# Kernel optimization log

Measured on AMD Instinct MI355X. Metric: run time of the kernel, lower is better.

## Reference

```python
import jax, jax.numpy as jnp
import numpy as np

N, E, G, ND, H, C, L = 100000, 640000, 1000, 128, 128, 10, 4
ATOMS_PER_GRAPH = 100  # N = G * ATOMS_PER_GRAPH
NEG_SLOPE = 0.01  # nn.LeakyReLU default


def setup_inputs() -> dict:
    key = jax.random.key(0)
    ks = jax.random.split(key, 16)
    s = 0.05
    return {
        "node_attr": jax.random.normal(ks[0], (N, ND), jnp.float32),
        "edge_index": jax.random.randint(ks[1], (2, E), 0, N, jnp.int64),
        "num_atoms": jnp.full((G,), ATOMS_PER_GRAPH, dtype=jnp.int64),
        "enc_W": jax.random.normal(ks[2], (ND, H), jnp.float32) * s,
        "enc_b": jnp.zeros((H,), jnp.float32),
        "gcn_W": jax.random.normal(ks[3], (L, H, H), jnp.float32) * s,
        "gcn_b": jnp.zeros((L, H), jnp.float32),
        "r_W1": jax.random.normal(ks[4], (H, H), jnp.float32) * s,
        "r_b1": jnp.zeros((H,), jnp.float32),
        "r_W2": jax.random.normal(ks[5], (H, H), jnp.float32) * s,
        "r_b2": jnp.zeros((H,), jnp.float32),
        "s_W1": jax.random.normal(ks[6], (H, H), jnp.float32) * s,
        "s_b1": jnp.zeros((H,), jnp.float32),
        "s_W2": jax.random.normal(ks[7], (H, H), jnp.float32) * s,
        "s_b2": jnp.zeros((H,), jnp.float32),
        "fin_W": jax.random.normal(ks[8], (H, C), jnp.float32) * s,
        "fin_b": jnp.zeros((C,), jnp.float32),
    }


def _leaky(x):
    return jnp.where(x > 0, x, NEG_SLOPE * x)


def reference(node_attr, edge_index, num_atoms, enc_W, enc_b, gcn_W, gcn_b,
              r_W1, r_b1, r_W2, r_b2, s_W1, s_b1, s_W2, s_b2, fin_W, fin_b):
    dst, src = edge_index[0], edge_index[1]
    # degree normalization constant across layers: deg(i) = in-edge count, divide by deg+1
    deg = jax.ops.segment_sum(jnp.ones((E,), node_attr.dtype), dst, num_segments=N)
    inv_deg = 1.0 / (deg + 1.0)  # [N]

    x = node_attr @ enc_W + enc_b  # [N, H]
    for l in range(L):
        h = x @ gcn_W[l] + gcn_b[l]
        agg = jax.ops.segment_sum(h[src], dst, num_segments=N)  # scatter_sum over dst
        x = (h + agg) * inv_deg[:, None]

    # GateMLP: ReLuMLP(x) * SigmoidMLP(x)
    r = _leaky(_leaky(x @ r_W1 + r_b1) @ r_W2 + r_b2)
    g = jax.nn.sigmoid(_leaky(x @ s_W1 + s_b1) @ s_W2 + s_b2)
    x = r * g  # [N, H]

    # graph pooling: scatter_mean over graph ids
    graph_mask = jnp.repeat(jnp.arange(G), num_atoms, total_repeat_length=N)
    gsum = jax.ops.segment_sum(x, graph_mask, num_segments=G)
    cnt = jax.ops.segment_sum(jnp.ones((N,), x.dtype), graph_mask, num_segments=G)
    graph_attr = gsum / jnp.maximum(cnt, 1.0)[:, None]  # [G, H]
    return graph_attr @ fin_W + fin_b  # [G, C]
```

## Files before the change

kernel.cpp:

```cpp
#include <hip/hip_runtime.h>
#include <hip/hip_bf16.h>
#include <cstddef>
#include <cstdint>

#define CAP 32
#define LEAK 0.01f

typedef __attribute__((ext_vector_type(8))) short short8v;
typedef __attribute__((ext_vector_type(4))) float float4v;

__device__ __forceinline__ unsigned short f2bf(float f) {
    uint32_t u = __float_as_uint(f);
    uint32_t r = (u + 0x7FFFu + ((u >> 16) & 1u)) >> 16;
    return (unsigned short)r;
}
__device__ __forceinline__ float bf2f(unsigned short s) {
    return __uint_as_float(((uint32_t)s) << 16);
}
__device__ __forceinline__ short8v frag_from_pairs(uint32_t p0, uint32_t p1,
                                                   uint32_t p2, uint32_t p3) {
    union { uint32_t u[4]; short8v v; } c;
    c.u[0] = p0; c.u[1] = p1; c.u[2] = p2; c.u[3] = p3;
    return c.v;
}

__global__ __launch_bounds__(256) void prep(const int* __restrict__ ei, int E_,
                                            int* __restrict__ cnt,
                                            int* __restrict__ bucket,
                                            const float* __restrict__ node_attr,
                                            unsigned short* __restrict__ bx, int Nn,
                                            const float* __restrict__ enc_W,
                                            const float* __restrict__ gcn_W,
                                            const float* __restrict__ rw1,
                                            const float* __restrict__ rw2,
                                            const float* __restrict__ sw1,
                                            const float* __restrict__ sw2,
                                            const float* __restrict__ enc_b,
                                            const float* __restrict__ gcn_b,
                                            const float* __restrict__ rb1,
                                            const float* __restrict__ sb1,
                                            unsigned short* __restrict__ wpack,
                                            float* __restrict__ fbias,
                                            const int* __restrict__ na,
                                            int* __restrict__ goff, int G_,
                                            int NB_EDGE, int NB_CVT) {
    const int b = blockIdx.x;
    const int tid = threadIdx.x;

    if (b < NB_EDGE) {
        int e = (b * 256 + tid) * 4;
        if (e >= E_) return;
        if (e + 4 <= E_) {
            int4 d4 = *(const int4*)&ei[e];
            int4 s4 = *(const int4*)&ei[(size_t)E_ + e];
            int p0 = atomicAdd(&cnt[d4.x], 1);
            int p1 = atomicAdd(&cnt[d4.y], 1);
            int p2 = atomicAdd(&cnt[d4.z], 1);
            int p3 = atomicAdd(&cnt[d4.w], 1);
            if (p0 < CAP) bucket[(size_t)d4.x * CAP + p0] = s4.x;
            if (p1 < CAP) bucket[(size_t)d4.y * CAP + p1] = s4.y;
            if (p2 < CAP) bucket[(size_t)d4.z * CAP + p2] = s4.z;
            if (p3 < CAP) bucket[(size_t)d4.w * CAP + p3] = s4.w;
        } else {
            for (; e < E_; ++e) {
                int d = ei[e], s = ei[(size_t)E_ + e];
                int p = atomicAdd(&cnt[d], 1);
                if (p < CAP) bucket[(size_t)d * CAP + p] = s;
            }
        }
        return;
    }
    if (b < NB_EDGE + NB_CVT) {
        size_t i8 = ((size_t)(b - NB_EDGE) * 256 + tid) * 8;
        if (i8 < (size_t)Nn * 128) {
            const float* ap = node_attr + i8;
            float4v p = *(const float4v*)ap;
            float4v q = *(const float4v*)(ap + 4);
            short8v v;
            v[0] = (short)f2bf(p[0]); v[1] = (short)f2bf(p[1]);
            v[2] = (short)f2bf(p[2]); v[3] = (short)f2bf(p[3]);
            v[4] = (short)f2bf(q[0]); v[5] = (short)f2bf(q[1]);
            v[6] = (short)f2bf(q[2]); v[7] = (short)f2bf(q[3]);
            *(short8v*)(bx + i8) = v;
        }
        return;
    }
    if (b < NB_EDGE + NB_CVT + 72) {
        int pb = b - (NB_EDGE + NB_CVT);
        int m = pb >> 3;
        if (m == 1) return;
        int idx = (pb & 7) * 256 + tid;
        const float* W;
        switch (m) {
            case 0: W = enc_W; break;
            case 2: case 3: case 4: W = gcn_W + (size_t)(m - 1) * 16384; break;
            case 5: W = rw1; break;
            case 6: W = rw2; break;
            case 7: W = sw1; break;
            default: W = sw2; break;
        }
        int n = idx & 127;
        int fg = (idx >> 7) & 3;
        int kc = idx >> 9;
        short8v v;
#pragma unroll
        for (int j = 0; j < 8; ++j)
            v[j] = (short)f2bf(W[(size_t)(kc * 32 + fg * 8 + j) * 128 + n]);
        *(short8v*)(wpack + (size_t)m * 16384 + (size_t)idx * 8) = v;
        return;
    }
    int fb = b - (NB_EDGE + NB_CVT + 72);
    if (fb < 192) {
        int which = fb / 64;
        int r = (fb % 64) * 2 + (tid >> 7);
        int n = tid & 127;
        const float* A = (which == 0) ? enc_W : gcn_W + (size_t)3 * 16384;
        const float* B = (which == 0) ? gcn_W : ((which == 1) ? rw1 : sw1);
        float acc = 0.f;
#pragma unroll 8
        for (int m2 = 0; m2 < 128; ++m2)
            acc = fmaf(A[(size_t)r * 128 + m2], B[(size_t)m2 * 128 + n], acc);
        int kc = r >> 5, fg2 = (r >> 3) & 3, j = r & 7;
        int sl = (which == 0) ? 1 : ((which == 1) ? 9 : 10);
        wpack[(size_t)sl * 16384 + (size_t)(((kc * 4 + fg2) * 128 + n) * 8 + j)] = f2bf(acc);
    } else if (fb < 195) {
        if (tid < 128) {
            int which = fb - 192;
            const float* B = (which == 0) ? gcn_W : ((which == 1) ? rw1 : sw1);
            const float* ba = (which == 0) ? enc_b : gcn_b + 384;
            const float* bb = (which == 0) ? gcn_b : ((which == 1) ? rb1 : sb1);
            float acc = bb[tid];
            for (int m2 = 0; m2 < 128; ++m2)
                acc = fmaf(ba[m2], B[(size_t)m2 * 128 + tid], acc);
            fbias[which * 128 + tid] = acc;
        }
    } else if (fb == 195) {
        __shared__ int sh[256];
        int base = tid * 4;
        int v0 = (base + 0 < G_) ? na[base + 0] : 0;
        int v1 = (base + 1 < G_) ? na[base + 1] : 0;
        int v2 = (base + 2 < G_) ? na[base + 2] : 0;
        int v3 = (base + 3 < G_) ? na[base + 3] : 0;
        int s = v0 + v1 + v2 + v3;
        sh[tid] = s;
        __syncthreads();
        for (int ofs = 1; ofs < 256; ofs <<= 1) {
            int u = (tid >= ofs) ? sh[tid - ofs] : 0;
            __syncthreads();
            sh[tid] += u;
            __syncthreads();
        }
        int run = sh[tid] - s;
        if (tid == 0) goff[0] = 0;
        run += v0; if (base + 0 < G_) goff[base + 1] = run;
        run += v1; if (base + 1 < G_) goff[base + 2] = run;
        run += v2; if (base + 2 < G_) goff[base + 3] = run;
        run += v3; if (base + 3 < G_) goff[base + 4] = run;
    }
}

__device__ __forceinline__ void load_wf(const unsigned short* __restrict__ Wpack,
                                        int w, int fr, int fg, short8v wf[2][4]) {
    const short8v* Wp = (const short8v*)Wpack;
#pragma unroll
    for (int t = 0; t < 2; ++t)
#pragma unroll
        for (int kc = 0; kc < 4; ++kc)
            wf[t][kc] = Wp[(kc * 4 + fg) * 128 + w * 32 + t * 16 + fr];
}

__device__ __forceinline__ void mfma_tile(const unsigned short* As, int fr, int fg,
                                          const short8v wf[2][4], float4v acc[4][2]) {
#pragma unroll
    for (int m = 0; m < 4; ++m) {
        acc[m][0] = (float4v){0.f, 0.f, 0.f, 0.f};
        acc[m][1] = (float4v){0.f, 0.f, 0.f, 0.f};
    }
#pragma unroll
    for (int kc = 0; kc < 4; ++kc) {
        short8v a[4];
#pragma unroll
        for (int m = 0; m < 4; ++m) {
            int row = m * 16 + fr;
            int cb = (kc * 64 + fg * 16) ^ ((row & 7) << 4);
            a[m] = *(const short8v*)((const char*)As + row * 256 + cb);
        }
#pragma unroll
        for (int m = 0; m < 4; ++m) {
            acc[m][0] = __builtin_amdgcn_mfma_f32_16x16x32_bf16(a[m], wf[0][kc], acc[m][0], 0, 0, 0);
            acc[m][1] = __builtin_amdgcn_mfma_f32_16x16x32_bf16(a[m], wf[1][kc], acc[m][1], 0, 0, 0);
        }
    }
}

__device__ __forceinline__ void acc8(float a[8], uint4 v, float m) {
    a[0] = fmaf(m, bf2f((unsigned short)(v.x & 0xffff)), a[0]);
    a[1] = fmaf(m, bf2f((unsigned short)(v.x >> 16)), a[1]);
    a[2] = fmaf(m, bf2f((unsigned short)(v.y & 0xffff)), a[2]);
    a[3] = fmaf(m, bf2f((unsigned short)(v.y >> 16)), a[3]);
    a[4] = fmaf(m, bf2f((unsigned short)(v.z & 0xffff)), a[4]);
    a[5] = fmaf(m, bf2f((unsigned short)(v.z >> 16)), a[5]);
    a[6] = fmaf(m, bf2f((unsigned short)(v.w & 0xffff)), a[6]);
    a[7] = fmaf(m, bf2f((unsigned short)(v.w >> 16)), a[7]);
}

__device__ __forceinline__ void issue4(const char* __restrict__ xb, int2 prep_,
                                       int gl, int l16, int Nn, int jb, uint4 V[4]) {
    const int sl = gl + (jb >> 1);
    int s0 = __shfl(prep_.x, sl);
    int s1 = __shfl(prep_.y, sl);
    int s2 = __shfl(prep_.x, sl + 1);
    int s3 = __shfl(prep_.y, sl + 1);
    s0 = min(max(s0, 0), Nn - 1);
    s1 = min(max(s1, 0), Nn - 1);
    s2 = min(max(s2, 0), Nn - 1);
    s3 = min(max(s3, 0), Nn - 1);
    V[0] = *(const uint4*)(xb + (size_t)s0 * 256 + l16 * 16);
    V[1] = *(const uint4*)(xb + (size_t)s1 * 256 + l16 * 16);
    V[2] = *(const uint4*)(xb + (size_t)s2 * 256 + l16 * 16);
    V[3] = *(const uint4*)(xb + (size_t)s3 * 256 + l16 * 16);
}

__device__ __forceinline__ void consume4(float a[8], const uint4 V[4], int jb, int d) {
    acc8(a, V[0], (jb + 0 < d) ? 1.f : 0.f);
    acc8(a, V[1], (jb + 1 < d) ? 1.f : 0.f);
    acc8(a, V[2], (jb + 2 < d) ? 1.f : 0.f);
    acc8(a, V[3], (jb + 3 < d) ? 1.f : 0.f);
}

template <bool AGGONLY>
__global__ __launch_bounds__(256, 4) void gcn_fused(const unsigned short* __restrict__ x,
                                                    const int* __restrict__ bucket,
                                                    const int* __restrict__ cnt,
                                                    const unsigned short* __restrict__ Wpack,
                                                    const float* __restrict__ bias,
                                                    unsigned short* __restrict__ xout,
                                                    int Nn) {
    __shared__ unsigned short As[64 * 128];
    const int tid = threadIdx.x;
    const int lane = tid & 63;
    const int w = tid >> 6;
    const int row0 = blockIdx.x * 64;
    const int fr = lane & 15;
    const int fg = lane >> 4;
    const int l16 = lane & 15;
    const int g = lane >> 4;
    const int gl = lane & 48;
    const char* xb = (const char*)x;

    int cfull = 0;
    if (lane < 16) {
        int gn = row0 + w * 16 + lane;
        if (gn >= Nn) gn = Nn - 1;
        cfull = cnt[gn];
    }
    uint4 own[4];
    int2 pre[4];
#pragma unroll
    for (int p = 0; p < 4; ++p) {
        int gn = row0 + w * 16 + p * 4 + g;
        if (gn >= Nn) gn = Nn - 1;
        own[p] = *(const uint4*)(xb + (size_t)gn * 256 + l16 * 16);
        pre[p] = *(const int2*)&bucket[(size_t)gn * CAP + 2 * l16];
    }

#pragma unroll
    for (int p = 0; p < 4; ++p) {
        const int n = p * 4 + g;
        const int r = w * 16 + n;
        const int dfull = __shfl(cfull, n);
        const float id = 1.0f / (float)(dfull + 1);
        const int d = min(dfull, CAP);

        uint4 VA[4], VB[4];
        issue4(xb, pre[p], gl, l16, Nn, 0, VA);

        float a[8];
        {
            uint4 o = own[p];
            a[0] = bf2f((unsigned short)(o.x & 0xffff));
            a[1] = bf2f((unsigned short)(o.x >> 16));
            a[2] = bf2f((unsigned short)(o.y & 0xffff));
            a[3] = bf2f((unsigned short)(o.y >> 16));
            a[4] = bf2f((unsigned short)(o.z & 0xffff));
            a[5] = bf2f((unsigned short)(o.z >> 16));
            a[6] = bf2f((unsigned short)(o.w & 0xffff));
            a[7] = bf2f((unsigned short)(o.w >> 16));
        }

        int j = 0;
        while (true) {
            if (j + 4 < d) issue4(xb, pre[p], gl, l16, Nn, j + 4, VB);
            consume4(a, VA, j, d);
            j += 4;
            if (j >= d) break;
            if (j + 4 < d) issue4(xb, pre[p], gl, l16, Nn, j + 4, VA);
            consume4(a, VB, j, d);
            j += 4;
            if (j >= d) break;
        }

#pragma unroll
        for (int i = 0; i < 8; ++i) a[i] *= id;
        uint4 o;
        o.x = (uint32_t)f2bf(a[0]) | ((uint32_t)f2bf(a[1]) << 16);
        o.y = (uint32_t)f2bf(a[2]) | ((uint32_t)f2bf(a[3]) << 16);
        o.z = (uint32_t)f2bf(a[4]) | ((uint32_t)f2bf(a[5]) << 16);
        o.w = (uint32_t)f2bf(a[6]) | ((uint32_t)f2bf(a[7]) << 16);
        if (AGGONLY) {
            int node = row0 + r;
            if (node < Nn)
                *(uint4*)((char*)xout + (size_t)node * 256 + l16 * 16) = o;
        } else {
            *(uint4*)((char*)As + r * 256 + ((l16 * 16) ^ ((r & 7) << 4))) = o;
        }
    }
    if (AGGONLY) return;

    short8v wf[2][4];
    load_wf(Wpack, w, fr, fg, wf);
    __syncthreads();

    float4v acc[4][2];
    mfma_tile(As, fr, fg, wf, acc);

#pragma unroll
    for (int t = 0; t < 2; ++t) {
        const int col = w * 32 + t * 16 + fr;
        const float bv = bias[col];
#pragma unroll
        for (int m = 0; m < 4; ++m)
#pragma unroll
            for (int q = 0; q < 4; ++q) {
                int row = row0 + m * 16 + fg * 4 + q;
                if (row < Nn) xout[(size_t)row * 128 + col] = f2bf(acc[m][t][q] + bv);
            }
    }
}

__global__ __launch_bounds__(512, 4) void gate_fused(const unsigned short* __restrict__ x,
                                                     const unsigned short* __restrict__ wpack,
                                                     const float* __restrict__ rb1f,
                                                     const float* __restrict__ rb2,
                                                     const float* __restrict__ sb1f,
                                                     const float* __restrict__ sb2,
                                                     unsigned short* __restrict__ out, int M) {
    __shared__ unsigned short Ws[2 * 128 * 128];
    const int tid = threadIdx.x;
    const int lane = tid & 63;
    const int w = tid >> 6;
    const int l16 = lane & 15;
    const int fg = lane >> 4;
    const int row0 = blockIdx.x * 128 + w * 16;

    int xr = row0 + l16;
    if (xr >= M) xr = M - 1;
    short8v xbf[4];
#pragma unroll
    for (int kc = 0; kc < 4; ++kc)
        xbf[kc] = *(const short8v*)(x + (size_t)xr * 128 + kc * 32 + fg * 8);

    const short8v* WL = (const short8v*)Ws;
    uint32_t upR[8][2], upS[8][2];

#define STAGE2(mi0, mi1)                                                      \
    {                                                                         \
        const short8v* s0 = (const short8v*)(wpack + (size_t)(mi0) * 16384);  \
        const short8v* s1 = (const short8v*)(wpack + (size_t)(mi1) * 16384);  \
        short8v* dst = (short8v*)Ws;                                          \
        _Pragma("unroll") for (int i = 0; i < 4; ++i)                         \
            dst[i * 512 + tid] = s0[i * 512 + tid];                          \
        _Pragma("unroll") for (int i = 0; i < 4; ++i)                         \
            dst[2048 + i * 512 + tid] = s1[i * 512 + tid];                    \
    }

#define PASS1(OFS, BIAS, UP)                                                  \
    _Pragma("unroll") for (int nt = 0; nt < 8; ++nt) {                        \
        float4v acc = (float4v){0.f, 0.f, 0.f, 0.f};                          \
        _Pragma("unroll") for (int kc = 0; kc < 4; ++kc)                      \
            acc = __builtin_amdgcn_mfma_f32_16x16x32_bf16(                    \
                WL[(OFS) + (kc * 4 + fg) * 128 + nt * 16 + l16], xbf[kc], acc, 0, 0, 0); \
        _Pragma("unroll") for (int q = 0; q < 4; ++q) {                       \
            float v = acc[q] + (BIAS)[nt * 16 + fg * 4 + q];                  \
            acc[q] = v > 0.f ? v : LEAK * v;                                  \
        }                                                                     \
        UP[nt][0] = (uint32_t)f2bf(acc[0]) | ((uint32_t)f2bf(acc[1]) << 16);  \
        UP[nt][1] = (uint32_t)f2bf(acc[2]) | ((uint32_t)f2bf(acc[3]) << 16);  \
    }

#define MKUF(UP, UF)                                                          \
    _Pragma("unroll") for (int kc = 0; kc < 4; ++kc) {                        \
        uint32_t pr0, pr1, pr2, pr3;                                          \
        {                                                                     \
            int srcl = (((2 * fg + 0) & 3) << 4) + l16;                       \
            uint32_t lo = __shfl((int)UP[2 * kc][0], srcl);                   \
            uint32_t hi = __shfl((int)UP[2 * kc + 1][0], srcl);               \
            pr0 = (fg & 2) ? hi : lo;                                         \
            lo = __shfl((int)UP[2 * kc][1], srcl);                            \
            hi = __shfl((int)UP[2 * kc + 1][1], srcl);                        \
            pr1 = (fg & 2) ? hi : lo;                                         \
        }                                                                     \
        {                                                                     \
            int srcl = (((2 * fg + 1) & 3) << 4) + l16;                       \
            uint32_t lo = __shfl((int)UP[2 * kc][0], srcl);                   \
            uint32_t hi = __shfl((int)UP[2 * kc + 1][0], srcl);               \
            pr2 = (fg & 2) ? hi : lo;                                         \
            lo = __shfl((int)UP[2 * kc][1], srcl);                            \
            hi = __shfl((int)UP[2 * kc + 1][1], srcl);                        \
            pr3 = (fg & 2) ? hi : lo;                                         \
        }                                                                     \
        UF[kc] = frag_from_pairs(pr0, pr1, pr2, pr3);                         \
    }

    STAGE2(9, 10);
    __syncthreads();
    PASS1(0, rb1f, upR);
    PASS1(2048, sb1f, upS);
    __syncthreads();

    STAGE2(6, 8);
    __syncthreads();

    short8v uf[4];
    MKUF(upR, uf);
    float4v rf[8];
#pragma unroll
    for (int t2 = 0; t2 < 8; ++t2) {
        float4v acc = (float4v){0.f, 0.f, 0.f, 0.f};
#pragma unroll
        for (int kc = 0; kc < 4; ++kc)
            acc = __builtin_amdgcn_mfma_f32_16x16x32_bf16(
                uf[kc], WL[(kc * 4 + fg) * 128 + t2 * 16 + l16], acc, 0, 0, 0);
        const float bv = rb2[t2 * 16 + l16];
#pragma unroll
        for (int q = 0; q < 4; ++q) {
            float v = acc[q] + bv;
            rf[t2][q] = v > 0.f ? v : LEAK * v;
        }
    }

    MKUF(upS, uf);
#pragma unroll
    for (int t2 = 0; t2 < 8; ++t2) {
        float4v acc = (float4v){0.f, 0.f, 0.f, 0.f};
#pragma unroll
        for (int kc = 0; kc < 4; ++kc)
            acc = __builtin_amdgcn_mfma_f32_16x16x32_bf16(
                uf[kc], WL[2048 + (kc * 4 + fg) * 128 + t2 * 16 + l16], acc, 0, 0, 0);
        const float bv = sb2[t2 * 16 + l16];
#pragma unroll
        for (int q = 0; q < 4; ++q) {
            int row = row0 + fg * 4 + q;
            if (row < M) {
                float gg = 1.f / (1.f + __expf(-(acc[q] + bv)));
                out[(size_t)row * 128 + t2 * 16 + l16] = f2bf(gg * rf[t2][q]);
            }
        }
    }
#undef STAGE2
#undef PASS1
#undef MKUF
}

__global__ void pool(const unsigned short* __restrict__ x, const int* __restrict__ goff,
                     float* __restrict__ gattr, int G_) {
    int g = blockIdx.x * 2 + (threadIdx.x >> 7);
    if (g >= G_) return;
    int d = threadIdx.x & 127;
    int a0 = goff[g], a1 = goff[g + 1];
    float s0 = 0.f, s1 = 0.f, s2 = 0.f, s3 = 0.f;
    int a = a0;
    for (; a + 4 <= a1; a += 4) {
        s0 += bf2f(x[(size_t)(a + 0) * 128 + d]);
        s1 += bf2f(x[(size_t)(a + 1) * 128 + d]);
        s2 += bf2f(x[(size_t)(a + 2) * 128 + d]);
        s3 += bf2f(x[(size_t)(a + 3) * 128 + d]);
    }
    for (; a < a1; ++a) s0 += bf2f(x[(size_t)a * 128 + d]);
    float s = (s0 + s1) + (s2 + s3);
    float c = (float)max(a1 - a0, 1);
    gattr[(size_t)g * 128 + d] = s / c;
}

__global__ void final_gemm(const float* __restrict__ gattr, const float* __restrict__ fW,
                           const float* __restrict__ fb, float* __restrict__ out,
                           int G_, int C_) {
    int i = blockIdx.x * 256 + threadIdx.x;
    if (i >= G_ * C_) return;
    int g = i / C_, c = i % C_;
    const float* row = gattr + (size_t)g * 128;
    float s = fb[c];
    for (int k = 0; k < 128; ++k) s = fmaf(row[k], fW[k * C_ + c], s);
    out[i] = s;
}

extern "C" void kernel_launch(void* const* d_in, const int* in_sizes, int n_in,
                              void* d_out, int out_size, void* d_ws, size_t ws_size,
                              hipStream_t stream) {
    const float* node_attr = (const float*)d_in[0];
    const int* edge_index  = (const int*)d_in[1];
    const int* num_atoms   = (const int*)d_in[2];
    const float* enc_W = (const float*)d_in[3];
    const float* enc_b = (const float*)d_in[4];
    const float* gcn_W = (const float*)d_in[5];
    const float* gcn_b = (const float*)d_in[6];
    const float* r_W1 = (const float*)d_in[7];
    const float* r_b1 = (const float*)d_in[8];
    const float* r_W2 = (const float*)d_in[9];
    const float* r_b2 = (const float*)d_in[10];
    const float* s_W1 = (const float*)d_in[11];
    const float* s_b1 = (const float*)d_in[12];
    const float* s_W2 = (const float*)d_in[13];
    const float* s_b2 = (const float*)d_in[14];
    const float* fin_W = (const float*)d_in[15];
    const float* fin_b = (const float*)d_in[16];
    float* out = (float*)d_out;

    const int N_ = in_sizes[0] / 128;
    const int E_ = in_sizes[1] / 2;
    const int G_ = in_sizes[2];
    const int C_ = in_sizes[16];

    size_t off = 0;
    auto alloc = [&](size_t bytes) -> void* {
        void* p = (char*)d_ws + off;
        off += (bytes + 255) & ~(size_t)255;
        return p;
    };
    unsigned short* bx = (unsigned short*)alloc((size_t)N_ * 128 * 2);
    unsigned short* bh = (unsigned short*)alloc((size_t)N_ * 128 * 2);
    int* bucket = (int*)alloc((size_t)N_ * CAP * 4);
    int* cnt    = (int*)alloc((size_t)N_ * 4);
    unsigned short* wpack = (unsigned short*)alloc((size_t)11 * 16384 * 2);
    float* fbias = (float*)alloc((size_t)3 * 128 * 4);
    int* goff   = (int*)alloc((size_t)(G_ + 1) * 4);
    float* gattr = (float*)alloc((size_t)G_ * 128 * 4);
    (void)ws_size; (void)n_in; (void)out_size;

    const int gemm_grid = (N_ + 63) / 64;
    const int NB_EDGE = (E_ / 4 + 255) / 256;
    const int NB_CVT = (N_ * 16 + 255) / 256;
    const int NB_PREP = NB_EDGE + NB_CVT + 72 + 196;

    hipMemsetAsync(cnt, 0, (size_t)N_ * 4, stream);
    prep<<<NB_PREP, 256, 0, stream>>>(edge_index, E_, cnt, bucket,
                                      node_attr, bx, N_,
                                      enc_W, gcn_W, r_W1, r_W2, s_W1, s_W2,
                                      enc_b, gcn_b, r_b1, s_b1,
                                      wpack, fbias, num_atoms, goff, G_,
                                      NB_EDGE, NB_CVT);

    gcn_fused<false><<<gemm_grid, 256, 0, stream>>>(bx, bucket, cnt,
                                                    wpack + (size_t)1 * 16384, fbias, bh, N_);
    gcn_fused<false><<<gemm_grid, 256, 0, stream>>>(bh, bucket, cnt,
                                                    wpack + (size_t)2 * 16384, gcn_b + 128, bx, N_);
    gcn_fused<false><<<gemm_grid, 256, 0, stream>>>(bx, bucket, cnt,
                                                    wpack + (size_t)3 * 16384, gcn_b + 256, bh, N_);
    gcn_fused<true><<<gemm_grid, 256, 0, stream>>>(bh, bucket, cnt,
                                                   nullptr, nullptr, bx, N_);

    gate_fused<<<(N_ + 127) / 128, 512, 0, stream>>>(bx, wpack, fbias + 128, r_b2,
                                                     fbias + 256, s_b2, bh, N_);

    pool<<<(G_ + 1) / 2, 256, 0, stream>>>(bh, goff, gattr, G_);
    final_gemm<<<(G_ * C_ + 255) / 256, 256, 0, stream>>>(gattr, fin_W, fin_b, out, G_, C_);
}
```

Before: 271.5 us.

## Fuse graph mean-pooling into gate MLP kernel via shared-memory atomics

After: 346.0 us. +27.5%, slower.

```diff
diff --git a/kernel.cpp b/kernel.cpp
--- a/kernel.cpp
+++ b/kernel.cpp
@@ -57,15 +57,15 @@
             int p1 = atomicAdd(&cnt[d4.y], 1);
             int p2 = atomicAdd(&cnt[d4.z], 1);
             int p3 = atomicAdd(&cnt[d4.w], 1);
-            if (p0 < CAP) bucket[(size_t)d4.x * CAP + p0] = s4.x;
-            if (p1 < CAP) bucket[(size_t)d4.y * CAP + p1] = s4.y;
-            if (p2 < CAP) bucket[(size_t)d4.z * CAP + p2] = s4.z;
-            if (p3 < CAP) bucket[(size_t)d4.w * CAP + p3] = s4.w;
+            if (p0 < CAP) __builtin_nontemporal_store(s4.x, &bucket[(size_t)d4.x * CAP + p0]);
+            if (p1 < CAP) __builtin_nontemporal_store(s4.y, &bucket[(size_t)d4.y * CAP + p1]);
+            if (p2 < CAP) __builtin_nontemporal_store(s4.z, &bucket[(size_t)d4.z * CAP + p2]);
+            if (p3 < CAP) __builtin_nontemporal_store(s4.w, &bucket[(size_t)d4.w * CAP + p3]);
         } else {
             for (; e < E_; ++e) {
                 int d = ei[e], s = ei[(size_t)E_ + e];
                 int p = atomicAdd(&cnt[d], 1);
-                if (p < CAP) bucket[(size_t)d * CAP + p] = s;
+                if (p < CAP) __builtin_nontemporal_store(s, &bucket[(size_t)d * CAP + p]);
             }
         }
         return;
@@ -344,14 +344,21 @@
                                                      const float* __restrict__ rb2,
                                                      const float* __restrict__ sb1f,
                                                      const float* __restrict__ sb2,
-                                                     unsigned short* __restrict__ out, int M) {
+                                                     const int* __restrict__ goff,
+                                                     float* __restrict__ gattr,
+                                                     int G_, int M) {
     __shared__ unsigned short Ws[2 * 128 * 128];
+    __shared__ float gs[4][128];
+    __shared__ int goffL[1025];
     const int tid = threadIdx.x;
     const int lane = tid & 63;
     const int w = tid >> 6;
     const int l16 = lane & 15;
     const int fg = lane >> 4;
     const int row0 = blockIdx.x * 128 + w * 16;
+
+    if (tid < 512) ((float*)gs)[tid] = 0.f;
+    for (int i = tid; i <= G_; i += 512) goffL[i] = goff[i];
 
     int xr = row0 + l16;
     if (xr >= M) xr = M - 1;
@@ -439,6 +446,27 @@
         }
     }
 
+    auto gsearch = [&](int r) {
+        int lo = 0, hi = G_ - 1;
+        while (lo < hi) {
+            int mid = (lo + hi + 1) >> 1;
+            if (goffL[mid] <= r) lo = mid; else hi = mid - 1;
+        }
+        return lo;
+    };
+    const int gfirst = gsearch(blockIdx.x * 128);
+    int gidx[4], gabs[4];
+    bool inl[4];
+#pragma unroll
+    for (int q = 0; q < 4; ++q) {
+        int row = row0 + fg * 4 + q;
+        int gg = gsearch(min(row, M - 1));
+        gabs[q] = gg;
+        int rel = gg - gfirst;
+        inl[q] = (rel >= 0 && rel < 4);
+        gidx[q] = rel & 3;
+    }
+
     MKUF(upS, uf);
 #pragma unroll
     for (int t2 = 0; t2 < 8; ++t2) {
@@ -448,13 +476,26 @@
             acc = __builtin_amdgcn_mfma_f32_16x16x32_bf16(
                 uf[kc], WL[2048 + (kc * 4 + fg) * 128 + t2 * 16 + l16], acc, 0, 0, 0);
         const float bv = sb2[t2 * 16 + l16];
+        const int c = t2 * 16 + l16;
 #pragma unroll
         for (int q = 0; q < 4; ++q) {
             int row = row0 + fg * 4 + q;
             if (row < M) {
                 float gg = 1.f / (1.f + __expf(-(acc[q] + bv)));
-                out[(size_t)row * 128 + t2 * 16 + l16] = f2bf(gg * rf[t2][q]);
+                float v = gg * rf[t2][q];
+                if (inl[q]) atomicAdd(&gs[gidx[q]][c], v);
+                else        atomicAdd(&gattr[(size_t)gabs[q] * 128 + c], v);
             }
+        }
+    }
+
+    __syncthreads();
+    {
+        int j = tid >> 7, c = tid & 127;
+        int gg = gfirst + j;
+        if (gg < G_) {
+            float v = gs[j][c];
+            if (v != 0.f) atomicAdd(&gattr[(size_t)gg * 128 + c], v);
         }
     }
 #undef STAGE2
@@ -462,36 +503,17 @@
 #undef MKUF
 }
 
-__global__ void pool(const unsigned short* __restrict__ x, const int* __restrict__ goff,
-                     float* __restrict__ gattr, int G_) {
-    int g = blockIdx.x * 2 + (threadIdx.x >> 7);
-    if (g >= G_) return;
-    int d = threadIdx.x & 127;
-    int a0 = goff[g], a1 = goff[g + 1];
-    float s0 = 0.f, s1 = 0.f, s2 = 0.f, s3 = 0.f;
-    int a = a0;
-    for (; a + 4 <= a1; a += 4) {
-        s0 += bf2f(x[(size_t)(a + 0) * 128 + d]);
-        s1 += bf2f(x[(size_t)(a + 1) * 128 + d]);
-        s2 += bf2f(x[(size_t)(a + 2) * 128 + d]);
-        s3 += bf2f(x[(size_t)(a + 3) * 128 + d]);
-    }
-    for (; a < a1; ++a) s0 += bf2f(x[(size_t)a * 128 + d]);
-    float s = (s0 + s1) + (s2 + s3);
-    float c = (float)max(a1 - a0, 1);
-    gattr[(size_t)g * 128 + d] = s / c;
-}
-
-__global__ void final_gemm(const float* __restrict__ gattr, const float* __restrict__ fW,
-                           const float* __restrict__ fb, float* __restrict__ out,
-                           int G_, int C_) {
+__global__ void final_gemm(const float* __restrict__ gattr, const int* __restrict__ goff,
+                           const float* __restrict__ fW, const float* __restrict__ fb,
+                           float* __restrict__ out, int G_, int C_) {
     int i = blockIdx.x * 256 + threadIdx.x;
     if (i >= G_ * C_) return;
     int g = i / C_, c = i % C_;
     const float* row = gattr + (size_t)g * 128;
-    float s = fb[c];
+    float s = 0.f;
     for (int k = 0; k < 128; ++k) s = fmaf(row[k], fW[k * C_ + c], s);
-    out[i] = s;
+    float cnt = (float)max(goff[g + 1] - goff[g], 1);
+    out[i] = s / cnt + fb[c];
 }
 
 extern "C" void kernel_launch(void* const* d_in, const int* in_sizes, int n_in,
@@ -543,6 +565,7 @@
     const int NB_PREP = NB_EDGE + NB_CVT + 72 + 196;
 
     hipMemsetAsync(cnt, 0, (size_t)N_ * 4, stream);
+    hipMemsetAsync(gattr, 0, (size_t)G_ * 128 * 4, stream);
     prep<<<NB_PREP, 256, 0, stream>>>(edge_index, E_, cnt, bucket,
                                       node_attr, bx, N_,
                                       enc_W, gcn_W, r_W1, r_W2, s_W1, s_W2,
@@ -560,8 +583,8 @@
                                                    nullptr, nullptr, bx, N_);
 
     gate_fused<<<(N_ + 127) / 128, 512, 0, stream>>>(bx, wpack, fbias + 128, r_b2,
-                                                     fbias + 256, s_b2, bh, N_);
-
-    pool<<<(G_ + 1) / 2, 256, 0, stream>>>(bh, goff, gattr, G_);
-    final_gemm<<<(G_ * C_ + 255) / 256, 256, 0, stream>>>(gattr, fin_W, fin_b, out, G_, C_);
-}
+                                                     fbias + 256, s_b2, goff, gattr, G_, N_);
+
+    final_gemm<<<(G_ * C_ + 255) / 256, 256, 0, stream>>>(gattr, goff, fin_W, fin_b,
+                                                          out, G_, C_);
+}
```
